# Kernel optimization log

Hardware: AMD Instinct MI355X
Metric: run time of the kernel (lower is better)

## Reference

```python
import math
import jax, jax.numpy as jnp
import numpy as np

D_MODEL = 1024
N_HEADS = 16
HEAD_DIM = D_MODEL // N_HEADS
ROPE_BASE = 10000.0
EPS = 1e-6


def rmsnorm(x, w, eps=EPS):
    # x: (..., head_dim); computed in fp32 like the torch code
    xf = x.astype(jnp.float32)
    rms = jax.lax.rsqrt(jnp.mean(xf * xf, axis=-1, keepdims=True) + eps)
    return (xf * rms).astype(x.dtype) * w


def apply_rope(x, cos, sin):
    # x: (B, H, T, head_dim); cos/sin: (T, head_dim/2)
    d2 = x.shape[-1] // 2
    x1, x2 = x[..., :d2], x[..., d2:]
    c = cos[None, None, :, :]
    s = sin[None, None, :, :]
    return jnp.concatenate([x1 * c - x2 * s, x2 * c + x1 * s], axis=-1)


def setup_inputs() -> dict:
    key = jax.random.key(0)
    ks = jax.random.split(key, 7)
    B, T = 2, 2048
    x = jax.random.normal(ks[0], (B, T, D_MODEL), dtype=jnp.float32)
    scale = 1.0 / math.sqrt(D_MODEL)
    Wq = jax.random.normal(ks[1], (D_MODEL, D_MODEL), dtype=jnp.float32) * scale
    Wk = jax.random.normal(ks[2], (D_MODEL, D_MODEL), dtype=jnp.float32) * scale
    Wv = jax.random.normal(ks[3], (D_MODEL, D_MODEL), dtype=jnp.float32) * scale
    Wo = jax.random.normal(ks[4], (D_MODEL, D_MODEL), dtype=jnp.float32) * scale
    q_norm_w = jnp.ones((HEAD_DIM,), dtype=jnp.float32)
    k_norm_w = jnp.ones((HEAD_DIM,), dtype=jnp.float32)
    return {"x": x, "Wq": Wq, "Wk": Wk, "Wv": Wv, "Wo": Wo,
            "q_norm_w": q_norm_w, "k_norm_w": k_norm_w}


def reference(x, Wq, Wk, Wv, Wo, q_norm_w, k_norm_w):
    B, T, d = x.shape
    H, hd = N_HEADS, HEAD_DIM
    # projections (nn.Linear applies x @ W.T; here W is stored as (in,out))
    q = (x @ Wq).reshape(B, T, H, hd).transpose(0, 2, 1, 3)  # (B,H,T,hd)
    k = (x @ Wk).reshape(B, T, H, hd).transpose(0, 2, 1, 3)
    v = (x @ Wv).reshape(B, T, H, hd).transpose(0, 2, 1, 3)
    # QK RMSNorm per head
    q = rmsnorm(q, q_norm_w)
    k = rmsnorm(k, k_norm_w)
    # rotary embeddings
    inv_freq = 1.0 / (ROPE_BASE ** (jnp.arange(0, hd, 2, dtype=jnp.float32) / hd))
    t = jnp.arange(T, dtype=jnp.float32)
    freqs = jnp.outer(t, inv_freq)  # (T, hd/2)
    cos, sin = jnp.cos(freqs), jnp.sin(freqs)
    q = apply_rope(q, cos, sin)
    k = apply_rope(k, cos, sin)
    # naive full attention with causal mask
    scale = 1.0 / math.sqrt(hd)
    attn = jnp.einsum('bhqd,bhkd->bhqk', q, k) * scale  # (B,H,T,T)
    causal = jnp.triu(jnp.full((T, T), -jnp.inf, dtype=attn.dtype), k=1)
    attn = attn + causal[None, None, :, :]
    attn = jax.nn.softmax(attn, axis=-1)
    out = jnp.einsum('bhqk,bhkd->bhqd', attn, v)
    out = out.transpose(0, 2, 1, 3).reshape(B, T, d)
    return out @ Wo
```

## Files before the change

kernel.cpp:

```cpp
#include <hip/hip_runtime.h>

typedef unsigned short u16;
typedef unsigned int   u32;
typedef __bf16 bf16x8 __attribute__((ext_vector_type(8)));
typedef float  f32x4  __attribute__((ext_vector_type(4)));
typedef float  f32x2  __attribute__((ext_vector_type(2)));
typedef u32    u32x4  __attribute__((ext_vector_type(4)));
typedef u16    u16x4  __attribute__((ext_vector_type(4)));

#define D_MODEL 1024
#define T_SEQ   2048
#define NH      16
#define HD      64

__device__ __forceinline__ float b2f(u16 u){ return __uint_as_float(((u32)u)<<16); }
__device__ __forceinline__ u16 f2b(float f){
  u32 x = __float_as_uint(f);
  x += 0x7fffu + ((x>>16)&1u);
  return (u16)(x>>16);
}

__device__ __forceinline__ void gll16(const void* g, void* l){
  __builtin_amdgcn_global_load_lds((const __attribute__((address_space(1))) unsigned int*)g,
                                   (__attribute__((address_space(3))) unsigned int*)l, 16, 0, 0);
}

__global__ __launch_bounds__(256) void f32_to_bf16(const float* __restrict__ src, u16* __restrict__ dst)
{
  const int i = (blockIdx.x*256 + threadIdx.x)<<2;
  f32x4 v = *(const f32x4*)(src + i);
  u16x4 o;
  o[0]=f2b(v[0]); o[1]=f2b(v[1]); o[2]=f2b(v[2]); o[3]=f2b(v[3]);
  *(u16x4*)(dst + i) = o;
}

__global__ void transpose_w(const float* __restrict__ W0, const float* __restrict__ W1,
                            const float* __restrict__ W2, const float* __restrict__ W3,
                            u16* __restrict__ T0, u16* __restrict__ T1,
                            u16* __restrict__ T2, u16* __restrict__ T3)
{
  __shared__ u16 s[32][33];
  const int z = blockIdx.z;
  const float* src = (z==0)?W0:(z==1)?W1:(z==2)?W2:W3;
  u16*         dst = (z==0)?T0:(z==1)?T1:(z==2)?T2:T3;
  const int x = threadIdx.x, y = threadIdx.y;
  const int r0 = blockIdx.y*32, c0 = blockIdx.x*32;
  #pragma unroll
  for (int r=0;r<4;r++) s[y + r*8][x] = f2b(src[(r0 + y + r*8)*D_MODEL + c0 + x]);
  __syncthreads();
  #pragma unroll
  for (int r=0;r<4;r++) dst[(c0 + y + r*8)*D_MODEL + r0 + x] = s[x][y + r*8];
}

__global__ __launch_bounds__(256) void rope_table(float* __restrict__ cs)
{
  const int gid = blockIdx.x*256 + threadIdx.x;
  const int t = gid >> 5, fi = gid & 31;
  const float invf = expf(-(float)fi * 0.2878231366242558f);
  float sn, cn;
  sincosf((float)t * invf, &sn, &cn);
  cs[gid*2]   = cn;
  cs[gid*2+1] = sn;
}

__global__ __launch_bounds__(256) void gemm_qkv(
    const u16* __restrict__ A, const u16* __restrict__ Bt,
    const float* __restrict__ qw, const float* __restrict__ kw,
    const float* __restrict__ cs,
    u16* __restrict__ Qb, u16* __restrict__ Kb, u16* __restrict__ Vt)
{
  __shared__ __align__(16) u16 sA[1024*8];
  __shared__ __align__(16) u16 sB[1024*8];
  const int id = blockIdx.x;
  const int xcd = id & 7, slot = id >> 3;
  const int bn = (xcd & 1)*12 + (slot % 12);
  const int bm = (xcd >> 1)*8 + (slot / 12);
  const int bm0 = bm<<7, bn0 = bn<<7;

  const int tid = threadIdx.x;
  const int lane = tid & 63;
  const int w  = tid>>6;
  const int wm = (w>>1)<<6;
  const int wn = (w&1)<<6;
  const int quad = lane>>4, lr = lane&15;
  const int swl = lr & 7;

  int rS[4], cS[4];
  #pragma unroll
  for (int i=0;i<4;i++){
    int s = i*256 + tid;
    rS[i] = s>>3;
    cS[i] = (s&7) ^ (rS[i]&7);
  }

  const f32x4 z4 = {0.f,0.f,0.f,0.f};
  f32x4 acc[4][4];
  #pragma unroll
  for (int i=0;i<4;i++)
    #pragma unroll
    for (int j=0;j<4;j++) acc[i][j] = z4;

  for (int kt=0; kt<D_MODEL; kt+=64){
    #pragma unroll
    for (int i=0;i<4;i++)
      gll16(A  + (bm0+rS[i])*D_MODEL + kt + cS[i]*8, sA + (i*256 + w*64)*8);
    #pragma unroll
    for (int i=0;i<4;i++)
      gll16(Bt + (bn0+rS[i])*D_MODEL + kt + cS[i]*8, sB + (i*256 + w*64)*8);
    __syncthreads();
    #pragma unroll
    for (int kk=0; kk<2; ++kk){
      bf16x8 af[4], bfr[4];
      const int cq = (kk*4 + quad) ^ swl;
      #pragma unroll
      for (int i=0;i<4;i++) af[i]  = *(const bf16x8*)(sA + ((wm + (i<<4) + lr)*8 + cq)*8);
      #pragma unroll
      for (int j=0;j<4;j++) bfr[j] = *(const bf16x8*)(sB + ((wn + (j<<4) + lr)*8 + cq)*8);
      #pragma unroll
      for (int i=0;i<4;i++)
        #pragma unroll
        for (int j=0;j<4;j++)
          acc[i][j] = __builtin_amdgcn_mfma_f32_16x16x32_bf16(af[i], bfr[j], acc[i][j], 0, 0, 0);
    }
    __syncthreads();
  }

  const int z = bn0 >> 10;
  const int ncl = bn0 & 1023;
  const int rq = quad<<2;

  if (z == 2){
    #pragma unroll
    for (int i=0;i<4;i++){
      int row0 = bm0 + wm + (i<<4) + rq;
      int bb = row0 >> 11, tt = row0 & (T_SEQ-1);
      #pragma unroll
      for (int j=0;j<4;j++){
        int nv = ncl + wn + (j<<4) + lr;
        int hh = nv >> 6, dd = nv & 63;
        u16x4 st;
        #pragma unroll
        for (int r=0;r<4;r++) st[r] = f2b(acc[i][j][r]);
        *(u16x4*)(Vt + ((bb*NH + hh)*HD + dd)*T_SEQ + tt) = st;
      }
    }
  } else {
    const float* w_ = (z==0) ? qw : kw;
    u16* dst = (z==0) ? Qb : Kb;
    const float scale = (z==0) ? 0.125f : 1.0f;
    float wv[4];
    #pragma unroll
    for (int j=0;j<4;j++) wv[j] = w_[(j<<4) + lr];
    #pragma unroll
    for (int i=0;i<4;i++){
      #pragma unroll
      for (int r=0;r<4;r++){
        const int grow = bm0 + wm + (i<<4) + rq + r;
        float ss = 0.f;
        #pragma unroll
        for (int j=0;j<4;j++) ss += acc[i][j][r]*acc[i][j][r];
        #pragma unroll
        for (int off=8; off>=1; off>>=1) ss += __shfl_xor(ss, off, 64);
        const float rms = rsqrtf(ss*(1.0f/64.0f) + 1e-6f);
        float xn[4];
        #pragma unroll
        for (int j=0;j<4;j++) xn[j] = acc[i][j][r]*rms*wv[j];
        const int t = grow & (T_SEQ-1);
        f32x2 c0 = *(const f32x2*)(cs + (t*32 + lr)*2);
        f32x2 c1 = *(const f32x2*)(cs + (t*32 + 16 + lr)*2);
        float o0 = xn[0]*c0[0] - xn[2]*c0[1];
        float o2 = xn[2]*c0[0] + xn[0]*c0[1];
        float o1 = xn[1]*c1[0] - xn[3]*c1[1];
        float o3 = xn[3]*c1[0] + xn[1]*c1[1];
        u16* rp = dst + grow*D_MODEL + ncl + wn + lr;
        rp[0]  = f2b(o0*scale);
        rp[16] = f2b(o1*scale);
        rp[32] = f2b(o2*scale);
        rp[48] = f2b(o3*scale);
      }
    }
  }
}

__global__ __launch_bounds__(256) void gemm_out(
    const u16* __restrict__ A, const u16* __restrict__ Bt, float* __restrict__ out)
{
  __shared__ __align__(16) u16 sA[1024*8];
  __shared__ __align__(16) u16 sB[1024*8];
  const int id = blockIdx.x;
  const int xcd = id & 7, slot = id >> 3;
  const int bn = slot & 7;
  const int bm = xcd*4 + (slot>>3);
  const int bm0 = bm<<7, bn0 = bn<<7;

  const int tid = threadIdx.x;
  const int lane = tid & 63;
  const int w  = tid>>6;
  const int wm = (w>>1)<<6;
  const int wn = (w&1)<<6;
  const int quad = lane>>4, lr = lane&15;
  const int swl = lr & 7;

  int rS[4], cS[4];
  #pragma unroll
  for (int i=0;i<4;i++){
    int s = i*256 + tid;
    rS[i] = s>>3;
    cS[i] = (s&7) ^ (rS[i]&7);
  }

  const f32x4 z4 = {0.f,0.f,0.f,0.f};
  f32x4 acc[4][4];
  #pragma unroll
  for (int i=0;i<4;i++)
    #pragma unroll
    for (int j=0;j<4;j++) acc[i][j] = z4;

  for (int kt=0; kt<D_MODEL; kt+=64){
    #pragma unroll
    for (int i=0;i<4;i++)
      gll16(A  + (bm0+rS[i])*D_MODEL + kt + cS[i]*8, sA + (i*256 + w*64)*8);
    #pragma unroll
    for (int i=0;i<4;i++)
      gll16(Bt + (bn0+rS[i])*D_MODEL + kt + cS[i]*8, sB + (i*256 + w*64)*8);
    __syncthreads();
    #pragma unroll
    for (int kk=0; kk<2; ++kk){
      bf16x8 af[4], bfr[4];
      const int cq = (kk*4 + quad) ^ swl;
      #pragma unroll
      for (int i=0;i<4;i++) af[i]  = *(const bf16x8*)(sA + ((wm + (i<<4) + lr)*8 + cq)*8);
      #pragma unroll
      for (int j=0;j<4;j++) bfr[j] = *(const bf16x8*)(sB + ((wn + (j<<4) + lr)*8 + cq)*8);
      #pragma unroll
      for (int i=0;i<4;i++)
        #pragma unroll
        for (int j=0;j<4;j++)
          acc[i][j] = __builtin_amdgcn_mfma_f32_16x16x32_bf16(af[i], bfr[j], acc[i][j], 0, 0, 0);
    }
    __syncthreads();
  }

  const int rq = quad<<2;
  #pragma unroll
  for (int i=0;i<4;i++){
    #pragma unroll
    for (int r=0;r<4;r++){
      const int grow = bm0 + wm + (i<<4) + rq + r;
      #pragma unroll
      for (int j=0;j<4;j++)
        out[grow*D_MODEL + bn0 + wn + (j<<4) + lr] = acc[i][j][r];
    }
  }
}

__global__ __launch_bounds__(256) void attn_mfma(const u16* __restrict__ Qb, const u16* __restrict__ Kb,
                                                 const u16* __restrict__ Vt, u16* __restrict__ AO)
{
  __shared__ __align__(16) u16 sK [2][512*8];
  __shared__ __align__(16) u16 sVT[2][512*8];
  __shared__ __align__(16) u16 sP [4][16*68];
  const int tid = threadIdx.x;
  const int h  = blockIdx.x, b = blockIdx.y;
  const int qt = 31 - blockIdx.z;
  const int w = tid>>6, lane = tid&63;
  const int quad = lane>>4, lr = lane&15;
  const int q8 = quad<<3;

  const int s0 = w*64 + lane, s1 = 256 + w*64 + lane;
  const int r0s = s0>>3, c0s = (s0&7)^(r0s&7);
  const int r1s = s1>>3, c1s = (s1&7)^(r1s&7);
  const u16* Kbase = Kb + (b*T_SEQ)*D_MODEL + h*HD;
  const u16* Vbase = Vt + (b*NH + h)*HD*T_SEQ;
  const int ldsOff0 = (w*64)*8, ldsOff1 = (256 + w*64)*8;

  const u16* Qrow = Qb + (b*T_SEQ + qt*64 + w*16 + lr)*D_MODEL + h*HD;
  bf16x8 qf0 = *(const bf16x8*)(Qrow + q8);
  bf16x8 qf1 = *(const bf16x8*)(Qrow + 32 + q8);

  f32x4 o[4];
  float lp[4];
  const f32x4 z4 = {0.f,0.f,0.f,0.f};
  const f32x4 i8 = {-8.f,-8.f,-8.f,-8.f};
  #pragma unroll
  for (int r=0;r<4;r++) lp[r] = 0.f;
  #pragma unroll
  for (int nt=0;nt<4;nt++) o[nt] = z4;

  u16* myP = sP[w];

  gll16(Kbase + r0s*D_MODEL + c0s*8, &sK[0][ldsOff0]);
  gll16(Kbase + r1s*D_MODEL + c1s*8, &sK[0][ldsOff1]);
  gll16(Vbase + r0s*T_SEQ + c0s*8,   &sVT[0][ldsOff0]);
  gll16(Vbase + r1s*T_SEQ + c1s*8,   &sVT[0][ldsOff1]);
  __syncthreads();

  for (int kt=0; kt<=qt; ++kt){
    const int cur = kt&1;
    if (kt < qt){
      const int kn = kt+1, nb = cur^1;
      gll16(Kbase + (kn*64 + r0s)*D_MODEL + c0s*8, &sK[nb][ldsOff0]);
      gll16(Kbase + (kn*64 + r1s)*D_MODEL + c1s*8, &sK[nb][ldsOff1]);
      gll16(Vbase + r0s*T_SEQ + kn*64 + c0s*8,     &sVT[nb][ldsOff0]);
      gll16(Vbase + r1s*T_SEQ + kn*64 + c1s*8,     &sVT[nb][ldsOff1]);
    }

    f32x4 s4[4];
    #pragma unroll
    for (int ct=0; ct<4; ++ct){
      const int row = ct*16 + lr;
      const int sw = row&7;
      bf16x8 k0 = *(const bf16x8*)(&sK[cur][(row*8 + (quad     ^ sw))*8]);
      bf16x8 k1 = *(const bf16x8*)(&sK[cur][(row*8 + ((4+quad) ^ sw))*8]);
      f32x4 acc = i8;
      acc = __builtin_amdgcn_mfma_f32_16x16x32_bf16(qf0, k0, acc, 0,0,0);
      acc = __builtin_amdgcn_mfma_f32_16x16x32_bf16(qf1, k1, acc, 0,0,0);
      s4[ct] = acc;
    }

    if (kt == qt){
      #pragma unroll
      for (int ct=0; ct<4; ++ct){
        int col = ct*16 + lr;
        #pragma unroll
        for (int r=0;r<4;r++)
          if (col > w*16 + quad*4 + r) s4[ct][r] = -1e30f;
      }
    }

    #pragma unroll
    for (int ct=0; ct<4; ++ct){
      #pragma unroll
      for (int r=0;r<4;r++){
        float p = __expf(s4[ct][r]);
        u32 pu = __float_as_uint(p) & 0xffff0000u;
        lp[r] += __uint_as_float(pu);
        myP[(quad*4 + r)*68 + ct*16 + lr] = (u16)(pu>>16);
      }
    }

    #pragma unroll
    for (int st=0; st<2; ++st){
      bf16x8 pf = *(const bf16x8*)(myP + lr*68 + st*32 + q8);
      #pragma unroll
      for (int nt=0;nt<4;nt++){
        const int row = nt*16 + lr;
        const int slot = row*8 + ((st*4+quad) ^ (row&7));
        bf16x8 vf = *(const bf16x8*)(&sVT[cur][slot*8]);
        o[nt] = __builtin_amdgcn_mfma_f32_16x16x32_bf16(pf, vf, o[nt], 0,0,0);
      }
    }
    __syncthreads();
  }

  #pragma unroll
  for (int r=0;r<4;r++){
    #pragma unroll
    for (int off=8; off>=1; off>>=1) lp[r] += __shfl_xor(lp[r], off, 64);
  }
  const int rowg = b*T_SEQ + qt*64 + w*16 + quad*4;
  #pragma unroll
  for (int r=0;r<4;r++){
    float inv = 1.0f / lp[r];
    #pragma unroll
    for (int nt=0;nt<4;nt++)
      AO[(rowg + r)*D_MODEL + h*HD + nt*16 + lr] = f2b(o[nt][r]*inv);
  }
}

extern "C" void kernel_launch(void* const* d_in, const int* in_sizes, int n_in,
                              void* d_out, int out_size, void* d_ws, size_t ws_size,
                              hipStream_t stream)
{
  const float* X  = (const float*)d_in[0];
  const float* Wq = (const float*)d_in[1];
  const float* Wk = (const float*)d_in[2];
  const float* Wv = (const float*)d_in[3];
  const float* Wo = (const float*)d_in[4];
  const float* qw = (const float*)d_in[5];
  const float* kw = (const float*)d_in[6];

  char* ws = (char*)d_ws;
  const size_t MB = 1024*1024;
  u16*   WqkvT = (u16*)(ws + 0*MB);
  u16*   WoT   = (u16*)(ws + 6*MB);
  u16*   Xb    = (u16*)(ws + 8*MB);
  u16*   Qb    = (u16*)(ws + 16*MB);
  u16*   Kb    = (u16*)(ws + 24*MB);
  u16*   Vt    = (u16*)(ws + 32*MB);
  u16*   AO    = (u16*)(ws + 40*MB);
  float* CS    = (float*)(ws + 48*MB);

  f32_to_bf16<<<dim3(4096), 256, 0, stream>>>(X, Xb);
  transpose_w<<<dim3(32,32,4), dim3(32,8), 0, stream>>>(
      Wq,Wk,Wv,Wo, WqkvT, WqkvT + 1024*1024, WqkvT + 2*1024*1024, WoT);
  rope_table<<<dim3(256), 256, 0, stream>>>(CS);
  gemm_qkv<<<dim3(768), 256, 0, stream>>>(Xb, WqkvT, qw, kw, CS, Qb, Kb, Vt);
  attn_mfma<<<dim3(NH, 2, 32), 256, 0, stream>>>(Qb, Kb, Vt, AO);
  gemm_out<<<dim3(256), 256, 0, stream>>>(AO, WoT, (float*)d_out);
}
```

Measured before the change: 204.4 us.

## Double attention query tile per wave, fuse prep kernels, use exp2 softmax

Attention blocks now cover 128 query rows, with each wave holding two 16-row Q fragments, so every K/V tile loaded into LDS feeds twice as many MFMAs. The grid is halved and block order is interleaved to balance the causal workload. The softmax uses exp2 with log2e folded into the Q scale, and the P staging buffer uses an XOR-swizzled layout with vector stores. The three prep kernels are merged into one launch, and the V store is permuted to match the new P layout. The cost is more registers per thread and a larger LDS footprint, which may lower occupancy, plus fewer blocks in flight for attention.

```diff
diff --git a/kernel.cpp b/kernel.cpp
--- a/kernel.cpp
+++ b/kernel.cpp
@@ -13,6 +13,9 @@
 #define NH      16
 #define HD      64
 
+#define QSCALE  0.18033688011112042f
+#define NEG8L2E -11.541560327111707f
+
 __device__ __forceinline__ float b2f(u16 u){ return __uint_as_float(((u32)u)<<16); }
 __device__ __forceinline__ u16 f2b(float f){
   u32 x = __float_as_uint(f);
@@ -25,42 +28,43 @@
                                    (__attribute__((address_space(3))) unsigned int*)l, 16, 0, 0);
 }
 
-__global__ __launch_bounds__(256) void f32_to_bf16(const float* __restrict__ src, u16* __restrict__ dst)
-{
-  const int i = (blockIdx.x*256 + threadIdx.x)<<2;
-  f32x4 v = *(const f32x4*)(src + i);
-  u16x4 o;
-  o[0]=f2b(v[0]); o[1]=f2b(v[1]); o[2]=f2b(v[2]); o[3]=f2b(v[3]);
-  *(u16x4*)(dst + i) = o;
-}
-
-__global__ void transpose_w(const float* __restrict__ W0, const float* __restrict__ W1,
-                            const float* __restrict__ W2, const float* __restrict__ W3,
-                            u16* __restrict__ T0, u16* __restrict__ T1,
-                            u16* __restrict__ T2, u16* __restrict__ T3)
+__global__ __launch_bounds__(256) void prep(
+    const float* __restrict__ X, u16* __restrict__ Xb,
+    const float* __restrict__ W0, const float* __restrict__ W1,
+    const float* __restrict__ W2, const float* __restrict__ W3,
+    u16* __restrict__ T0, u16* __restrict__ T1,
+    u16* __restrict__ T2, u16* __restrict__ T3,
+    float* __restrict__ cs)
 {
   __shared__ u16 s[32][33];
-  const int z = blockIdx.z;
-  const float* src = (z==0)?W0:(z==1)?W1:(z==2)?W2:W3;
-  u16*         dst = (z==0)?T0:(z==1)?T1:(z==2)?T2:T3;
-  const int x = threadIdx.x, y = threadIdx.y;
-  const int r0 = blockIdx.y*32, c0 = blockIdx.x*32;
-  #pragma unroll
-  for (int r=0;r<4;r++) s[y + r*8][x] = f2b(src[(r0 + y + r*8)*D_MODEL + c0 + x]);
-  __syncthreads();
-  #pragma unroll
-  for (int r=0;r<4;r++) dst[(c0 + y + r*8)*D_MODEL + r0 + x] = s[x][y + r*8];
-}
-
-__global__ __launch_bounds__(256) void rope_table(float* __restrict__ cs)
-{
-  const int gid = blockIdx.x*256 + threadIdx.x;
-  const int t = gid >> 5, fi = gid & 31;
-  const float invf = expf(-(float)fi * 0.2878231366242558f);
-  float sn, cn;
-  sincosf((float)t * invf, &sn, &cn);
-  cs[gid*2]   = cn;
-  cs[gid*2+1] = sn;
+  const int id = blockIdx.x, tid = threadIdx.x;
+  if (id < 4096){
+    const int i = (id*256 + tid)<<2;
+    f32x4 v = *(const f32x4*)(X + i);
+    u16x4 o;
+    o[0]=f2b(v[0]); o[1]=f2b(v[1]); o[2]=f2b(v[2]); o[3]=f2b(v[3]);
+    *(u16x4*)(Xb + i) = o;
+  } else if (id < 8192){
+    const int wid = id - 4096;
+    const int z = wid >> 10, tile = wid & 1023;
+    const float* src = (z==0)?W0:(z==1)?W1:(z==2)?W2:W3;
+    u16*         dst = (z==0)?T0:(z==1)?T1:(z==2)?T2:T3;
+    const int x = tid & 31, y = tid >> 5;
+    const int r0 = (tile>>5)*32, c0 = (tile&31)*32;
+    #pragma unroll
+    for (int r=0;r<4;r++) s[y + r*8][x] = f2b(src[(r0 + y + r*8)*D_MODEL + c0 + x]);
+    __syncthreads();
+    #pragma unroll
+    for (int r=0;r<4;r++) dst[(c0 + y + r*8)*D_MODEL + r0 + x] = s[x][y + r*8];
+  } else {
+    const int gid = (id-8192)*256 + tid;
+    const int t = gid >> 5, fi = gid & 31;
+    const float invf = expf(-(float)fi * 0.2878231366242558f);
+    float sn, cn;
+    sincosf((float)t * invf, &sn, &cn);
+    cs[gid*2]   = cn;
+    cs[gid*2+1] = sn;
+  }
 }
 
 __global__ __launch_bounds__(256) void gemm_qkv(
@@ -138,16 +142,19 @@
       for (int j=0;j<4;j++){
         int nv = ncl + wn + (j<<4) + lr;
         int hh = nv >> 6, dd = nv & 63;
-        u16x4 st;
-        #pragma unroll
-        for (int r=0;r<4;r++) st[r] = f2b(acc[i][j][r]);
-        *(u16x4*)(Vt + ((bb*NH + hh)*HD + dd)*T_SEQ + tt) = st;
+        u16* basep = Vt + ((bb*NH + hh)*HD + dd)*T_SEQ;
+        #pragma unroll
+        for (int r=0;r<4;r++){
+          int t = tt + r;
+          int pt = (t & ~63) + ((t&15)<<2) + ((t>>4)&3);
+          basep[pt] = f2b(acc[i][j][r]);
+        }
       }
     }
   } else {
     const float* w_ = (z==0) ? qw : kw;
     u16* dst = (z==0) ? Qb : Kb;
-    const float scale = (z==0) ? 0.125f : 1.0f;
+    const float scale = (z==0) ? QSCALE : 1.0f;
     float wv[4];
     #pragma unroll
     for (int j=0;j<4;j++) wv[j] = w_[(j<<4) + lr];
@@ -257,12 +264,13 @@
 __global__ __launch_bounds__(256) void attn_mfma(const u16* __restrict__ Qb, const u16* __restrict__ Kb,
                                                  const u16* __restrict__ Vt, u16* __restrict__ AO)
 {
-  __shared__ __align__(16) u16 sK [2][512*8];
-  __shared__ __align__(16) u16 sVT[2][512*8];
-  __shared__ __align__(16) u16 sP [4][16*68];
+  __shared__ __align__(16) u16 sK [2][4096];
+  __shared__ __align__(16) u16 sVT[2][4096];
+  __shared__ __align__(16) u16 sP [4][2048];
   const int tid = threadIdx.x;
   const int h  = blockIdx.x, b = blockIdx.y;
-  const int qt = 31 - blockIdx.z;
+  const int zb = blockIdx.z;
+  const int qt = (zb < 8) ? (15 - zb) : (zb - 8);
   const int w = tid>>6, lane = tid&63;
   const int quad = lane>>4, lr = lane&15;
   const int q8 = quad<<3;
@@ -274,20 +282,29 @@
   const u16* Vbase = Vt + (b*NH + h)*HD*T_SEQ;
   const int ldsOff0 = (w*64)*8, ldsOff1 = (256 + w*64)*8;
 
-  const u16* Qrow = Qb + (b*T_SEQ + qt*64 + w*16 + lr)*D_MODEL + h*HD;
-  bf16x8 qf0 = *(const bf16x8*)(Qrow + q8);
-  bf16x8 qf1 = *(const bf16x8*)(Qrow + 32 + q8);
-
-  f32x4 o[4];
-  float lp[4];
+  bf16x8 qf[2][2];
+  #pragma unroll
+  for (int s=0;s<2;s++){
+    const u16* Qrow = Qb + (b*T_SEQ + qt*128 + w*32 + s*16 + lr)*D_MODEL + h*HD;
+    qf[s][0] = *(const bf16x8*)(Qrow + q8);
+    qf[s][1] = *(const bf16x8*)(Qrow + 32 + q8);
+  }
+
+  f32x4 o[2][4];
+  float lp[2][4];
   const f32x4 z4 = {0.f,0.f,0.f,0.f};
-  const f32x4 i8 = {-8.f,-8.f,-8.f,-8.f};
-  #pragma unroll
-  for (int r=0;r<4;r++) lp[r] = 0.f;
-  #pragma unroll
-  for (int nt=0;nt<4;nt++) o[nt] = z4;
+  const f32x4 ci = {NEG8L2E, NEG8L2E, NEG8L2E, NEG8L2E};
+  #pragma unroll
+  for (int s=0;s<2;s++)
+    #pragma unroll
+    for (int r=0;r<4;r++){ lp[s][r] = 0.f; }
+  #pragma unroll
+  for (int s=0;s<2;s++)
+    #pragma unroll
+    for (int nt=0;nt<4;nt++) o[s][nt] = z4;
 
   u16* myP = sP[w];
+  const int nk = 2*qt + 2;
 
   gll16(Kbase + r0s*D_MODEL + c0s*8, &sK[0][ldsOff0]);
   gll16(Kbase + r1s*D_MODEL + c1s*8, &sK[0][ldsOff1]);
@@ -295,9 +312,9 @@
   gll16(Vbase + r1s*T_SEQ + c1s*8,   &sVT[0][ldsOff1]);
   __syncthreads();
 
-  for (int kt=0; kt<=qt; ++kt){
+  for (int kt=0; kt<nk; ++kt){
     const int cur = kt&1;
-    if (kt < qt){
+    if (kt+1 < nk){
       const int kn = kt+1, nb = cur^1;
       gll16(Kbase + (kn*64 + r0s)*D_MODEL + c0s*8, &sK[nb][ldsOff0]);
       gll16(Kbase + (kn*64 + r1s)*D_MODEL + c1s*8, &sK[nb][ldsOff1]);
@@ -305,66 +322,92 @@
       gll16(Vbase + r1s*T_SEQ + kn*64 + c1s*8,     &sVT[nb][ldsOff1]);
     }
 
-    f32x4 s4[4];
+    f32x4 s4[2][4];
     #pragma unroll
     for (int ct=0; ct<4; ++ct){
       const int row = ct*16 + lr;
       const int sw = row&7;
       bf16x8 k0 = *(const bf16x8*)(&sK[cur][(row*8 + (quad     ^ sw))*8]);
       bf16x8 k1 = *(const bf16x8*)(&sK[cur][(row*8 + ((4+quad) ^ sw))*8]);
-      f32x4 acc = i8;
-      acc = __builtin_amdgcn_mfma_f32_16x16x32_bf16(qf0, k0, acc, 0,0,0);
-      acc = __builtin_amdgcn_mfma_f32_16x16x32_bf16(qf1, k1, acc, 0,0,0);
-      s4[ct] = acc;
-    }
-
-    if (kt == qt){
+      #pragma unroll
+      for (int s=0;s<2;s++){
+        f32x4 acc = ci;
+        acc = __builtin_amdgcn_mfma_f32_16x16x32_bf16(qf[s][0], k0, acc, 0,0,0);
+        acc = __builtin_amdgcn_mfma_f32_16x16x32_bf16(qf[s][1], k1, acc, 0,0,0);
+        s4[s][ct] = acc;
+      }
+    }
+
+    if (kt >= nk-2){
       #pragma unroll
       for (int ct=0; ct<4; ++ct){
-        int col = ct*16 + lr;
-        #pragma unroll
-        for (int r=0;r<4;r++)
-          if (col > w*16 + quad*4 + r) s4[ct][r] = -1e30f;
-      }
-    }
-
-    #pragma unroll
-    for (int ct=0; ct<4; ++ct){
+        const int colg = kt*64 + ct*16 + lr;
+        #pragma unroll
+        for (int s=0;s<2;s++){
+          const int rowb = qt*128 + w*32 + s*16 + quad*4;
+          #pragma unroll
+          for (int r=0;r<4;r++)
+            if (colg > rowb + r) s4[s][ct][r] = -1e30f;
+        }
+      }
+    }
+
+    #pragma unroll
+    for (int s=0;s<2;s++){
       #pragma unroll
       for (int r=0;r<4;r++){
-        float p = __expf(s4[ct][r]);
-        u32 pu = __float_as_uint(p) & 0xffff0000u;
-        lp[r] += __uint_as_float(pu);
-        myP[(quad*4 + r)*68 + ct*16 + lr] = (u16)(pu>>16);
+        u16x4 pk;
+        #pragma unroll
+        for (int ct=0; ct<4; ++ct){
+          float p = exp2f(s4[s][ct][r]);
+          u32 pu = __float_as_uint(p) & 0xffff0000u;
+          lp[s][r] += __uint_as_float(pu);
+          pk[ct] = (u16)(pu>>16);
+        }
+        const int prow = s*16 + quad*4 + r;
+        const int pidx = prow*64 + (((lr>>1) ^ (prow&7))<<3) + ((lr&1)<<2);
+        *(u16x4*)(myP + pidx) = pk;
       }
     }
 
     #pragma unroll
     for (int st=0; st<2; ++st){
-      bf16x8 pf = *(const bf16x8*)(myP + lr*68 + st*32 + q8);
+      bf16x8 pf[2];
+      #pragma unroll
+      for (int s=0;s<2;s++){
+        const int prow = s*16 + lr;
+        pf[s] = *(const bf16x8*)(myP + prow*64 + (((st*4+quad) ^ (lr&7))<<3));
+      }
       #pragma unroll
       for (int nt=0;nt<4;nt++){
         const int row = nt*16 + lr;
-        const int slot = row*8 + ((st*4+quad) ^ (row&7));
-        bf16x8 vf = *(const bf16x8*)(&sVT[cur][slot*8]);
-        o[nt] = __builtin_amdgcn_mfma_f32_16x16x32_bf16(pf, vf, o[nt], 0,0,0);
-      }
-    }
-    __syncthreads();
-  }
-
-  #pragma unroll
-  for (int r=0;r<4;r++){
-    #pragma unroll
-    for (int off=8; off>=1; off>>=1) lp[r] += __shfl_xor(lp[r], off, 64);
-  }
-  const int rowg = b*T_SEQ + qt*64 + w*16 + quad*4;
-  #pragma unroll
-  for (int r=0;r<4;r++){
-    float inv = 1.0f / lp[r];
-    #pragma unroll
-    for (int nt=0;nt<4;nt++)
-      AO[(rowg + r)*D_MODEL + h*HD + nt*16 + lr] = f2b(o[nt][r]*inv);
+        const int slotv = row*8 + ((st*4+quad) ^ (row&7));
+        bf16x8 vf = *(const bf16x8*)(&sVT[cur][slotv*8]);
+        #pragma unroll
+        for (int s=0;s<2;s++)
+          o[s][nt] = __builtin_amdgcn_mfma_f32_16x16x32_bf16(pf[s], vf, o[s][nt], 0,0,0);
+      }
+    }
+    __syncthreads();
+  }
+
+  #pragma unroll
+  for (int s=0;s<2;s++)
+    #pragma unroll
+    for (int r=0;r<4;r++){
+      #pragma unroll
+      for (int off=8; off>=1; off>>=1) lp[s][r] += __shfl_xor(lp[s][r], off, 64);
+    }
+  #pragma unroll
+  for (int s=0;s<2;s++){
+    const int rowg = b*T_SEQ + qt*128 + w*32 + s*16 + quad*4;
+    #pragma unroll
+    for (int r=0;r<4;r++){
+      float inv = 1.0f / lp[s][r];
+      #pragma unroll
+      for (int nt=0;nt<4;nt++)
+        AO[(rowg + r)*D_MODEL + h*HD + nt*16 + lr] = f2b(o[s][nt][r]*inv);
+    }
   }
 }
 
@@ -391,11 +434,9 @@
   u16*   AO    = (u16*)(ws + 40*MB);
   float* CS    = (float*)(ws + 48*MB);
 
-  f32_to_bf16<<<dim3(4096), 256, 0, stream>>>(X, Xb);
-  transpose_w<<<dim3(32,32,4), dim3(32,8), 0, stream>>>(
-      Wq,Wk,Wv,Wo, WqkvT, WqkvT + 1024*1024, WqkvT + 2*1024*1024, WoT);
-  rope_table<<<dim3(256), 256, 0, stream>>>(CS);
+  prep<<<dim3(8448), 256, 0, stream>>>(X, Xb, Wq, Wk, Wv, Wo,
+      WqkvT, WqkvT + 1024*1024, WqkvT + 2*1024*1024, WoT, CS);
   gemm_qkv<<<dim3(768), 256, 0, stream>>>(Xb, WqkvT, qw, kw, CS, Qb, Kb, Vt);
-  attn_mfma<<<dim3(NH, 2, 32), 256, 0, stream>>>(Qb, Kb, Vt, AO);
+  attn_mfma<<<dim3(NH, 2, 16), 256, 0, stream>>>(Qb, Kb, Vt, AO);
   gemm_out<<<dim3(256), 256, 0, stream>>>(AO, WoT, (float*)d_out);
 }
```

After: 209.3 us. +2.4%, slower.

## Fuse prep kernels, exp2 softmax, swizzled P buffer, permuted V layout, smaller out tiles

Applied to the files above, without the earlier changes.

Merges the three preprocessing kernels (bf16 cast, weight transpose, rope table) into one launch to cut launch overhead. Folds log2(e) into the Q scale and the softmax offset so attention can use exp2f. P is written as packed 4-element vectors into an XOR-swizzled 64-wide LDS buffer instead of scalar stores into a padded one. V is stored with tokens permuted within each 64 block so each lane's P fragment lines up with its V fragment. The output GEMM uses 64x128 tiles over 512 blocks to raise occupancy, at the cost of strided scalar V stores in the QKV epilogue.

```diff
diff --git a/kernel.cpp b/kernel.cpp
--- a/kernel.cpp
+++ b/kernel.cpp
@@ -13,6 +13,9 @@
 #define NH      16
 #define HD      64
 
+#define QSCALE  0.18033688011112042f
+#define NEG8L2E -11.541560327111707f
+
 __device__ __forceinline__ float b2f(u16 u){ return __uint_as_float(((u32)u)<<16); }
 __device__ __forceinline__ u16 f2b(float f){
   u32 x = __float_as_uint(f);
@@ -25,42 +28,43 @@
                                    (__attribute__((address_space(3))) unsigned int*)l, 16, 0, 0);
 }
 
-__global__ __launch_bounds__(256) void f32_to_bf16(const float* __restrict__ src, u16* __restrict__ dst)
-{
-  const int i = (blockIdx.x*256 + threadIdx.x)<<2;
-  f32x4 v = *(const f32x4*)(src + i);
-  u16x4 o;
-  o[0]=f2b(v[0]); o[1]=f2b(v[1]); o[2]=f2b(v[2]); o[3]=f2b(v[3]);
-  *(u16x4*)(dst + i) = o;
-}
-
-__global__ void transpose_w(const float* __restrict__ W0, const float* __restrict__ W1,
-                            const float* __restrict__ W2, const float* __restrict__ W3,
-                            u16* __restrict__ T0, u16* __restrict__ T1,
-                            u16* __restrict__ T2, u16* __restrict__ T3)
+__global__ __launch_bounds__(256) void prep(
+    const float* __restrict__ X, u16* __restrict__ Xb,
+    const float* __restrict__ W0, const float* __restrict__ W1,
+    const float* __restrict__ W2, const float* __restrict__ W3,
+    u16* __restrict__ T0, u16* __restrict__ T1,
+    u16* __restrict__ T2, u16* __restrict__ T3,
+    float* __restrict__ cs)
 {
   __shared__ u16 s[32][33];
-  const int z = blockIdx.z;
-  const float* src = (z==0)?W0:(z==1)?W1:(z==2)?W2:W3;
-  u16*         dst = (z==0)?T0:(z==1)?T1:(z==2)?T2:T3;
-  const int x = threadIdx.x, y = threadIdx.y;
-  const int r0 = blockIdx.y*32, c0 = blockIdx.x*32;
-  #pragma unroll
-  for (int r=0;r<4;r++) s[y + r*8][x] = f2b(src[(r0 + y + r*8)*D_MODEL + c0 + x]);
-  __syncthreads();
-  #pragma unroll
-  for (int r=0;r<4;r++) dst[(c0 + y + r*8)*D_MODEL + r0 + x] = s[x][y + r*8];
-}
-
-__global__ __launch_bounds__(256) void rope_table(float* __restrict__ cs)
-{
-  const int gid = blockIdx.x*256 + threadIdx.x;
-  const int t = gid >> 5, fi = gid & 31;
-  const float invf = expf(-(float)fi * 0.2878231366242558f);
-  float sn, cn;
-  sincosf((float)t * invf, &sn, &cn);
-  cs[gid*2]   = cn;
-  cs[gid*2+1] = sn;
+  const int id = blockIdx.x, tid = threadIdx.x;
+  if (id < 4096){
+    const int i = (id*256 + tid)<<2;
+    f32x4 v = *(const f32x4*)(X + i);
+    u16x4 o;
+    o[0]=f2b(v[0]); o[1]=f2b(v[1]); o[2]=f2b(v[2]); o[3]=f2b(v[3]);
+    *(u16x4*)(Xb + i) = o;
+  } else if (id < 8192){
+    const int wid = id - 4096;
+    const int z = wid >> 10, tile = wid & 1023;
+    const float* src = (z==0)?W0:(z==1)?W1:(z==2)?W2:W3;
+    u16*         dst = (z==0)?T0:(z==1)?T1:(z==2)?T2:T3;
+    const int x = tid & 31, y = tid >> 5;
+    const int r0 = (tile>>5)*32, c0 = (tile&31)*32;
+    #pragma unroll
+    for (int r=0;r<4;r++) s[y + r*8][x] = f2b(src[(r0 + y + r*8)*D_MODEL + c0 + x]);
+    __syncthreads();
+    #pragma unroll
+    for (int r=0;r<4;r++) dst[(c0 + y + r*8)*D_MODEL + r0 + x] = s[x][y + r*8];
+  } else {
+    const int gid = (id-8192)*256 + tid;
+    const int t = gid >> 5, fi = gid & 31;
+    const float invf = expf(-(float)fi * 0.2878231366242558f);
+    float sn, cn;
+    sincosf((float)t * invf, &sn, &cn);
+    cs[gid*2]   = cn;
+    cs[gid*2+1] = sn;
+  }
 }
 
 __global__ __launch_bounds__(256) void gemm_qkv(
@@ -138,16 +142,19 @@
       for (int j=0;j<4;j++){
         int nv = ncl + wn + (j<<4) + lr;
         int hh = nv >> 6, dd = nv & 63;
-        u16x4 st;
-        #pragma unroll
-        for (int r=0;r<4;r++) st[r] = f2b(acc[i][j][r]);
-        *(u16x4*)(Vt + ((bb*NH + hh)*HD + dd)*T_SEQ + tt) = st;
+        u16* basep = Vt + ((bb*NH + hh)*HD + dd)*T_SEQ;
+        #pragma unroll
+        for (int r=0;r<4;r++){
+          int t = tt + r;
+          int pt = (t & ~63) + ((t&15)<<2) + ((t>>4)&3);
+          basep[pt] = f2b(acc[i][j][r]);
+        }
       }
     }
   } else {
     const float* w_ = (z==0) ? qw : kw;
     u16* dst = (z==0) ? Qb : Kb;
-    const float scale = (z==0) ? 0.125f : 1.0f;
+    const float scale = (z==0) ? QSCALE : 1.0f;
     float wv[4];
     #pragma unroll
     for (int j=0;j<4;j++) wv[j] = w_[(j<<4) + lr];
@@ -185,18 +192,18 @@
 __global__ __launch_bounds__(256) void gemm_out(
     const u16* __restrict__ A, const u16* __restrict__ Bt, float* __restrict__ out)
 {
-  __shared__ __align__(16) u16 sA[1024*8];
+  __shared__ __align__(16) u16 sA[512*8];
   __shared__ __align__(16) u16 sB[1024*8];
   const int id = blockIdx.x;
   const int xcd = id & 7, slot = id >> 3;
+  const int bm = xcd*8 + (slot>>3);
   const int bn = slot & 7;
-  const int bm = xcd*4 + (slot>>3);
-  const int bm0 = bm<<7, bn0 = bn<<7;
+  const int bm0 = bm<<6, bn0 = bn<<7;
 
   const int tid = threadIdx.x;
   const int lane = tid & 63;
   const int w  = tid>>6;
-  const int wm = (w>>1)<<6;
+  const int wm = (w>>1)<<5;
   const int wn = (w&1)<<6;
   const int quad = lane>>4, lr = lane&15;
   const int swl = lr & 7;
@@ -210,15 +217,15 @@
   }
 
   const f32x4 z4 = {0.f,0.f,0.f,0.f};
-  f32x4 acc[4][4];
-  #pragma unroll
-  for (int i=0;i<4;i++)
+  f32x4 acc[2][4];
+  #pragma unroll
+  for (int i=0;i<2;i++)
     #pragma unroll
     for (int j=0;j<4;j++) acc[i][j] = z4;
 
   for (int kt=0; kt<D_MODEL; kt+=64){
     #pragma unroll
-    for (int i=0;i<4;i++)
+    for (int i=0;i<2;i++)
       gll16(A  + (bm0+rS[i])*D_MODEL + kt + cS[i]*8, sA + (i*256 + w*64)*8);
     #pragma unroll
     for (int i=0;i<4;i++)
@@ -226,14 +233,14 @@
     __syncthreads();
     #pragma unroll
     for (int kk=0; kk<2; ++kk){
-      bf16x8 af[4], bfr[4];
+      bf16x8 af[2], bfr[4];
       const int cq = (kk*4 + quad) ^ swl;
       #pragma unroll
-      for (int i=0;i<4;i++) af[i]  = *(const bf16x8*)(sA + ((wm + (i<<4) + lr)*8 + cq)*8);
+      for (int i=0;i<2;i++) af[i]  = *(const bf16x8*)(sA + ((wm + (i<<4) + lr)*8 + cq)*8);
       #pragma unroll
       for (int j=0;j<4;j++) bfr[j] = *(const bf16x8*)(sB + ((wn + (j<<4) + lr)*8 + cq)*8);
       #pragma unroll
-      for (int i=0;i<4;i++)
+      for (int i=0;i<2;i++)
         #pragma unroll
         for (int j=0;j<4;j++)
           acc[i][j] = __builtin_amdgcn_mfma_f32_16x16x32_bf16(af[i], bfr[j], acc[i][j], 0, 0, 0);
@@ -243,7 +250,7 @@
 
   const int rq = quad<<2;
   #pragma unroll
-  for (int i=0;i<4;i++){
+  for (int i=0;i<2;i++){
     #pragma unroll
     for (int r=0;r<4;r++){
       const int grow = bm0 + wm + (i<<4) + rq + r;
@@ -257,9 +264,9 @@
 __global__ __launch_bounds__(256) void attn_mfma(const u16* __restrict__ Qb, const u16* __restrict__ Kb,
                                                  const u16* __restrict__ Vt, u16* __restrict__ AO)
 {
-  __shared__ __align__(16) u16 sK [2][512*8];
-  __shared__ __align__(16) u16 sVT[2][512*8];
-  __shared__ __align__(16) u16 sP [4][16*68];
+  __shared__ __align__(16) u16 sK [2][4096];
+  __shared__ __align__(16) u16 sVT[2][4096];
+  __shared__ __align__(16) u16 sP [4][1024];
   const int tid = threadIdx.x;
   const int h  = blockIdx.x, b = blockIdx.y;
   const int qt = 31 - blockIdx.z;
@@ -281,7 +288,7 @@
   f32x4 o[4];
   float lp[4];
   const f32x4 z4 = {0.f,0.f,0.f,0.f};
-  const f32x4 i8 = {-8.f,-8.f,-8.f,-8.f};
+  const f32x4 ci = {NEG8L2E, NEG8L2E, NEG8L2E, NEG8L2E};
   #pragma unroll
   for (int r=0;r<4;r++) lp[r] = 0.f;
   #pragma unroll
@@ -312,7 +319,7 @@
       const int sw = row&7;
       bf16x8 k0 = *(const bf16x8*)(&sK[cur][(row*8 + (quad     ^ sw))*8]);
       bf16x8 k1 = *(const bf16x8*)(&sK[cur][(row*8 + ((4+quad) ^ sw))*8]);
-      f32x4 acc = i8;
+      f32x4 acc = ci;
       acc = __builtin_amdgcn_mfma_f32_16x16x32_bf16(qf0, k0, acc, 0,0,0);
       acc = __builtin_amdgcn_mfma_f32_16x16x32_bf16(qf1, k1, acc, 0,0,0);
       s4[ct] = acc;
@@ -329,24 +336,28 @@
     }
 
     #pragma unroll
-    for (int ct=0; ct<4; ++ct){
-      #pragma unroll
-      for (int r=0;r<4;r++){
-        float p = __expf(s4[ct][r]);
+    for (int r=0;r<4;r++){
+      u16x4 pk;
+      #pragma unroll
+      for (int ct=0; ct<4; ++ct){
+        float p = exp2f(s4[ct][r]);
         u32 pu = __float_as_uint(p) & 0xffff0000u;
         lp[r] += __uint_as_float(pu);
-        myP[(quad*4 + r)*68 + ct*16 + lr] = (u16)(pu>>16);
+        pk[ct] = (u16)(pu>>16);
       }
+      const int prow = quad*4 + r;
+      const int pidx = prow*64 + (((lr>>1) ^ (prow&7))<<3) + ((lr&1)<<2);
+      *(u16x4*)(myP + pidx) = pk;
     }
 
     #pragma unroll
     for (int st=0; st<2; ++st){
-      bf16x8 pf = *(const bf16x8*)(myP + lr*68 + st*32 + q8);
+      bf16x8 pf = *(const bf16x8*)(myP + lr*64 + (((st*4+quad) ^ (lr&7))<<3));
       #pragma unroll
       for (int nt=0;nt<4;nt++){
         const int row = nt*16 + lr;
-        const int slot = row*8 + ((st*4+quad) ^ (row&7));
-        bf16x8 vf = *(const bf16x8*)(&sVT[cur][slot*8]);
+        const int slotv = row*8 + ((st*4+quad) ^ (row&7));
+        bf16x8 vf = *(const bf16x8*)(&sVT[cur][slotv*8]);
         o[nt] = __builtin_amdgcn_mfma_f32_16x16x32_bf16(pf, vf, o[nt], 0,0,0);
       }
     }
@@ -391,11 +402,9 @@
   u16*   AO    = (u16*)(ws + 40*MB);
   float* CS    = (float*)(ws + 48*MB);
 
-  f32_to_bf16<<<dim3(4096), 256, 0, stream>>>(X, Xb);
-  transpose_w<<<dim3(32,32,4), dim3(32,8), 0, stream>>>(
-      Wq,Wk,Wv,Wo, WqkvT, WqkvT + 1024*1024, WqkvT + 2*1024*1024, WoT);
-  rope_table<<<dim3(256), 256, 0, stream>>>(CS);
+  prep<<<dim3(8448), 256, 0, stream>>>(X, Xb, Wq, Wk, Wv, Wo,
+      WqkvT, WqkvT + 1024*1024, WqkvT + 2*1024*1024, WoT, CS);
   gemm_qkv<<<dim3(768), 256, 0, stream>>>(Xb, WqkvT, qw, kw, CS, Qb, Kb, Vt);
   attn_mfma<<<dim3(NH, 2, 32), 256, 0, stream>>>(Qb, Kb, Vt, AO);
-  gemm_out<<<dim3(256), 256, 0, stream>>>(AO, WoT, (float*)d_out);
-}
+  gemm_out<<<dim3(512), 256, 0, stream>>>(AO, WoT, (float*)d_out);
+}
```

Result: faster. 185.9 us (-9.0%).
